# Kernel tuning notes

Hardware: AMD Instinct MI355X
Metric: run time of the kernel (lower is better)

## Reference

```python
import jax, jax.numpy as jnp
import numpy as np

N_EMBD = 768
N_HEAD = 12
HEAD_DIM = N_EMBD // N_HEAD  # 64


def setup_inputs() -> dict:
    key = jax.random.key(0)
    k1, k2, k3 = jax.random.split(key, 3)
    B, S = 4, 2048
    x = jax.random.normal(k1, (B, S, N_EMBD), dtype=jnp.float32)
    W_attn = jax.random.normal(k2, (N_EMBD, 3 * N_EMBD), dtype=jnp.float32) * 0.02
    b_attn = jax.random.normal(k3, (3 * N_EMBD,), dtype=jnp.float32) * 0.02
    return {"x": x, "W_attn": W_attn, "b_attn": b_attn}


def reference(x, W_attn, b_attn):
    B, S, E = x.shape
    H, D = N_HEAD, HEAD_DIM
    # fused QKV projection (torch Linear: x @ W^T + b; here W_attn stored as [E, 3E])
    qkv = x @ W_attn + b_attn  # [B, S, 3E]
    q, k, v = jnp.split(qkv, 3, axis=-1)
    q = q.reshape(B, S, H, D)
    k = k.reshape(B, S, H, D)
    v = v.reshape(B, S, H, D)
    scale = 1.0 / np.sqrt(D).astype(np.float32)
    scores = jnp.einsum('bqhd,bkhd->bhqk', q, k) * scale  # [B, H, S, S]
    causal = jnp.tril(jnp.ones((S, S), dtype=bool))
    # ReLU attention nonlinearity (no softmax); masked entries -> 0
    att = jnp.where(causal, jnp.maximum(scores, 0.0), 0.0)
    y = jnp.einsum('bhqk,bkhd->bqhd', att, v)  # [B, S, H, D]
    return y.reshape(B, S, E)
```

## Files before the change

### kernel.cpp

```cpp
#include <hip/hip_runtime.h>

typedef __attribute__((ext_vector_type(8))) short short8;
typedef __attribute__((ext_vector_type(4))) short short4v;
typedef __attribute__((ext_vector_type(4))) float floatx4;
typedef __attribute__((ext_vector_type(2))) unsigned int uint2v;

#define S_LEN 2048
#define NH 12
#define HD 64
#define EMB 768
#define E3 2304
#define N_ITEMS 768

__device__ __forceinline__ unsigned short f2bf(float f) {
    unsigned int u = __builtin_bit_cast(unsigned int, f);
    u += 0x7FFFu + ((u >> 16) & 1u);
    return (unsigned short)(u >> 16);
}

__device__ __forceinline__ unsigned int pack2bf(float a, float b) {
#if __has_builtin(__builtin_amdgcn_cvt_pk_bf16_f32)
    typedef __attribute__((ext_vector_type(2))) short short2v;
    short2v r = __builtin_amdgcn_cvt_pk_bf16_f32(a, b);
    return __builtin_bit_cast(unsigned int, r);
#else
    return (unsigned int)f2bf(a) | ((unsigned int)f2bf(b) << 16);
#endif
}

__device__ __forceinline__ void gl_lds16(const void* g, void* l) {
    __builtin_amdgcn_global_load_lds(
        (const __attribute__((address_space(1))) unsigned int*)g,
        (__attribute__((address_space(3))) unsigned int*)l, 16, 0, 0);
}

__global__ __launch_bounds__(256) void conv_x(const float* __restrict__ x,
                                              ushort* __restrict__ xb,
                                              int* __restrict__ counter) {
    if (blockIdx.x == 0 && threadIdx.x == 0) *counter = 0;
    int i = (blockIdx.x * 256 + threadIdx.x) * 4;
    float4 f = *(const float4*)(x + i);
    ushort4 o;
    o.x = f2bf(f.x); o.y = f2bf(f.y); o.z = f2bf(f.z); o.w = f2bf(f.w);
    *(ushort4*)(xb + i) = o;
}

__global__ __launch_bounds__(256) void conv_w(const float* __restrict__ W,
                                              ushort* __restrict__ Wt) {
    __shared__ float tile[32][33];
    int n0 = blockIdx.x * 32, k0 = blockIdx.y * 32;
    int tx = threadIdx.x, ty = threadIdx.y;
    for (int i = 0; i < 4; i++)
        tile[ty + i * 8][tx] = W[(size_t)(k0 + ty + i * 8) * E3 + n0 + tx];
    __syncthreads();
    for (int i = 0; i < 4; i++)
        Wt[(size_t)(n0 + ty + i * 8) * EMB + k0 + tx] = f2bf(tile[tx][ty + i * 8]);
}

__global__ __launch_bounds__(256) void qkv_gemm(const ushort* __restrict__ Xb,
                                                const ushort* __restrict__ Wt,
                                                const float* __restrict__ bias,
                                                ushort* __restrict__ Q,
                                                ushort* __restrict__ K,
                                                ushort* __restrict__ Vt) {
    __shared__ ushort Ald[128 * 64];
    __shared__ ushort Bld[128 * 64];
    int tid  = threadIdx.x;
    int wv = tid >> 6, lane = tid & 63;
    int l15 = lane & 15, quad = lane >> 4;
    int r8 = lane >> 3, cc = lane & 7;
    int wm = wv >> 1, wn = wv & 1;
    int m0 = blockIdx.x * 128, n0 = blockIdx.y * 128;

    floatx4 acc[4][4] = {};

    for (int k0 = 0; k0 < EMB; k0 += 64) {
        __syncthreads();
        for (int i = 0; i < 4; i++) {
            int row = wv * 32 + i * 8 + r8;
            int gc  = cc ^ r8;
            gl_lds16(Xb + (size_t)(m0 + row) * EMB + k0 + gc * 8,
                     (char*)Ald + (wv * 32 + i * 8) * 128);
            gl_lds16(Wt + (size_t)(n0 + row) * EMB + k0 + gc * 8,
                     (char*)Bld + (wv * 32 + i * 8) * 128);
        }
        __syncthreads();
        for (int ch = 0; ch < 2; ch++) {
            int sw = ((ch * 4 + quad) ^ (l15 & 7)) * 16;
            short8 af[4], bf[4];
            for (int mi = 0; mi < 4; mi++)
                af[mi] = *(const short8*)((const char*)Ald + (wm * 64 + mi * 16 + l15) * 128 + sw);
            for (int ni = 0; ni < 4; ni++)
                bf[ni] = *(const short8*)((const char*)Bld + (wn * 64 + ni * 16 + l15) * 128 + sw);
            for (int mi = 0; mi < 4; mi++)
                for (int ni = 0; ni < 4; ni++)
                    acc[mi][ni] = __builtin_amdgcn_mfma_f32_16x16x32_bf16(
                        af[mi], bf[ni], acc[mi][ni], 0, 0, 0);
        }
    }

    int seg = n0 / EMB;
    for (int ni = 0; ni < 4; ni++) {
        int n = n0 + wn * 64 + ni * 16 + l15;
        float bv = bias[n];
        int nn = n - seg * EMB;
        int h = nn >> 6, d = nn & 63;
        for (int mi = 0; mi < 4; mi++) {
            for (int r = 0; r < 4; r++) {
                int m = m0 + wm * 64 + mi * 16 + quad * 4 + r;
                int b = m >> 11, s = m & 2047;
                ushort v = f2bf(acc[mi][ni][r] + bv);
                if (seg == 0)
                    Q[(((size_t)b * NH + h) * S_LEN + s) * HD + d] = v;
                else if (seg == 1)
                    K[(((size_t)b * NH + h) * S_LEN + s) * HD + d] = v;
                else
                    Vt[(((size_t)b * NH + h) * HD + d) * S_LEN + s] = v;
            }
        }
    }
}

__global__ __launch_bounds__(256) void attn(const ushort* __restrict__ Q,
                                            const ushort* __restrict__ K,
                                            const ushort* __restrict__ Vt,
                                            float* __restrict__ out,
                                            int* __restrict__ counter) {
    __shared__ ushort Kld[2][64 * 64];
    __shared__ ushort Vld[2][64 * 64];
    __shared__ int s_item;
    int tid = threadIdx.x;
    int w = tid >> 6, lane = tid & 63;
    int l15 = lane & 15, quad = lane >> 4;
    int r8 = lane >> 3, cc = lane & 7;

    while (true) {
        if (tid == 0) s_item = atomicAdd(counter, 1);
        __syncthreads();
        int it = s_item;
        __syncthreads();
        if (it >= N_ITEMS) break;
        int qt = 15 - it / 48;
        int bh = it % 48;

        const ushort* Qbase = Q + ((size_t)bh * S_LEN + qt * 128) * HD;
        const ushort* Kbase = K + (size_t)bh * S_LEN * HD;
        const ushort* Vbase = Vt + (size_t)bh * HD * S_LEN;

        short8 qf[2][2];
        for (int nq = 0; nq < 2; nq++)
            for (int ch = 0; ch < 2; ch++)
                qf[nq][ch] = *(const short8*)(Qbase + (size_t)(w * 32 + nq * 16 + l15) * HD
                                              + ch * 32 + quad * 8);

        floatx4 acco[2][4] = {};
        int njt = 2 * qt + 2;

        {
            const ushort* Kt = Kbase;
            const ushort* Vb = Vbase;
            for (int i = 0; i < 2; i++) {
                int row = w * 16 + i * 8 + r8;
                int gc  = cc ^ r8;
                gl_lds16(Kt + (size_t)row * HD + gc * 8,
                         (char*)Kld[0] + (w * 16 + i * 8) * 128);
                gl_lds16(Vb + (size_t)row * S_LEN + gc * 8,
                         (char*)Vld[0] + (w * 16 + i * 8) * 128);
            }
        }
        int p = 0;
        for (int jt = 0; jt < njt; jt++) {
            __syncthreads();
            if (jt + 1 < njt) {
                const ushort* Kt = Kbase + (size_t)(jt + 1) * 64 * HD;
                const ushort* Vb = Vbase + (size_t)(jt + 1) * 64;
                for (int i = 0; i < 2; i++) {
                    int row = w * 16 + i * 8 + r8;
                    int gc  = cc ^ r8;
                    gl_lds16(Kt + (size_t)row * HD + gc * 8,
                             (char*)Kld[p ^ 1] + (w * 16 + i * 8) * 128);
                    gl_lds16(Vb + (size_t)row * S_LEN + gc * 8,
                             (char*)Vld[p ^ 1] + (w * 16 + i * 8) * 128);
                }
            }

            floatx4 st[4][2] = {};
            for (int ch = 0; ch < 2; ch++) {
                int sw = ((ch * 4 + quad) ^ (l15 & 7)) * 16;
                short8 kf[4];
                for (int mk = 0; mk < 4; mk++)
                    kf[mk] = *(const short8*)((const char*)Kld[p] + (mk * 16 + l15) * 128 + sw);
                for (int mk = 0; mk < 4; mk++)
                    for (int nq = 0; nq < 2; nq++)
                        st[mk][nq] = __builtin_amdgcn_mfma_f32_16x16x32_bf16(
                            kf[mk], qf[nq][ch], st[mk][nq], 0, 0, 0);
            }

            unsigned int pk[4][2][2];
            bool diag = (jt >= 2 * qt);
            for (int mk = 0; mk < 4; mk++) {
                for (int nq = 0; nq < 2; nq++) {
                    float e[4];
                    for (int r = 0; r < 4; r++)
                        e[r] = fmaxf(st[mk][nq][r] * 0.125f, 0.0f);
                    if (diag) {
                        int kg = jt * 64 + mk * 16 + quad * 4;
                        int qg = qt * 128 + w * 32 + nq * 16 + l15;
                        for (int r = 0; r < 4; r++)
                            if (kg + r > qg) e[r] = 0.0f;
                    }
                    pk[mk][nq][0] = pack2bf(e[0], e[1]);
                    pk[mk][nq][1] = pack2bf(e[2], e[3]);
                }
            }

            for (int mk = 0; mk < 4; mk++) {
                short4v vf[4];
                for (int ni = 0; ni < 4; ni++) {
                    int c2 = (mk * 2 + (quad >> 1)) ^ (l15 & 7);
                    vf[ni] = *(const short4v*)((const char*)Vld[p] + (ni * 16 + l15) * 128
                                               + c2 * 16 + (quad & 1) * 8);
                }
                for (int mi = 0; mi < 2; mi++) {
                    short4v a = __builtin_bit_cast(short4v,
                                 (uint2v){pk[mk][mi][0], pk[mk][mi][1]});
                    for (int ni = 0; ni < 4; ni++)
                        acco[mi][ni] = __builtin_amdgcn_mfma_f32_16x16x16bf16_1k(
                            a, vf[ni], acco[mi][ni], 0, 0, 0);
                }
            }
            p ^= 1;
        }

        int b = bh / NH, h = bh % NH;
        for (int mi = 0; mi < 2; mi++) {
            for (int ni = 0; ni < 4; ni++) {
                int d = ni * 16 + l15;
                for (int r = 0; r < 4; r++) {
                    int s = qt * 128 + w * 32 + mi * 16 + quad * 4 + r;
                    out[((size_t)(b * S_LEN + s)) * EMB + h * HD + d] = acco[mi][ni][r];
                }
            }
        }
        __syncthreads();
    }
}

extern "C" void kernel_launch(void* const* d_in, const int* in_sizes, int n_in,
                              void* d_out, int out_size, void* d_ws, size_t ws_size,
                              hipStream_t stream) {
    const float* x    = (const float*)d_in[0];
    const float* W    = (const float*)d_in[1];
    const float* bias = (const float*)d_in[2];
    float* out = (float*)d_out;

    char* ws = (char*)d_ws;
    const size_t SZ_X = (size_t)8192 * EMB * 2;
    const size_t SZ_W = (size_t)E3 * EMB * 2;
    const size_t SZ_H = (size_t)4 * NH * S_LEN * HD * 2;
    ushort* Xb = (ushort*)(ws);
    ushort* Wt = (ushort*)(ws + SZ_X);
    ushort* Qb = (ushort*)(ws + SZ_X + SZ_W);
    ushort* Kb = (ushort*)(ws + SZ_X + SZ_W + SZ_H);
    ushort* Vt = (ushort*)(ws + SZ_X + SZ_W + 2 * SZ_H);
    int* counter = (int*)(ws + SZ_X + SZ_W + 3 * SZ_H);

    conv_x<<<dim3(8192 * EMB / (256 * 4)), dim3(256), 0, stream>>>(x, Xb, counter);
    conv_w<<<dim3(E3 / 32, EMB / 32), dim3(32, 8), 0, stream>>>(W, Wt);
    qkv_gemm<<<dim3(64, 18), dim3(256), 0, stream>>>(Xb, Wt, bias, Qb, Kb, Vt);
    attn<<<dim3(512), dim3(256), 0, stream>>>(Qb, Kb, Vt, out, counter);
}
```

Before: 202.8 us.

## Fuse conversion kernels, stage GEMM epilogue through LDS, use 128-key attention tiles

Merges the x and W bf16 conversion kernels into one launch. The QKV GEMM epilogue now goes through LDS so it can write coalesced 16-byte stores, with Q pre-scaled by 1/8 into a token-major QK buffer and V transposed per tile. The attention loop processes 128-key stages with larger double-buffered K/V tiles, halving the barrier count, and reads Q and K straight from the row-major QK buffer with a stride of 1536. The cost is more LDS per block, which may lower occupancy, and strided global reads for K.

After: 187.6 us. 1.08x faster.

```diff
diff --git a/kernel.cpp b/kernel.cpp
--- a/kernel.cpp
+++ b/kernel.cpp
@@ -34,37 +34,40 @@
         (__attribute__((address_space(3))) unsigned int*)l, 16, 0, 0);
 }
 
-__global__ __launch_bounds__(256) void conv_x(const float* __restrict__ x,
-                                              ushort* __restrict__ xb,
-                                              int* __restrict__ counter) {
-    if (blockIdx.x == 0 && threadIdx.x == 0) *counter = 0;
-    int i = (blockIdx.x * 256 + threadIdx.x) * 4;
-    float4 f = *(const float4*)(x + i);
-    ushort4 o;
-    o.x = f2bf(f.x); o.y = f2bf(f.y); o.z = f2bf(f.z); o.w = f2bf(f.w);
-    *(ushort4*)(xb + i) = o;
-}
-
-__global__ __launch_bounds__(256) void conv_w(const float* __restrict__ W,
-                                              ushort* __restrict__ Wt) {
-    __shared__ float tile[32][33];
-    int n0 = blockIdx.x * 32, k0 = blockIdx.y * 32;
-    int tx = threadIdx.x, ty = threadIdx.y;
-    for (int i = 0; i < 4; i++)
-        tile[ty + i * 8][tx] = W[(size_t)(k0 + ty + i * 8) * E3 + n0 + tx];
-    __syncthreads();
-    for (int i = 0; i < 4; i++)
-        Wt[(size_t)(n0 + ty + i * 8) * EMB + k0 + tx] = f2bf(tile[tx][ty + i * 8]);
+__global__ __launch_bounds__(256) void conv_fused(const float* __restrict__ x,
+                                                  ushort* __restrict__ xb,
+                                                  const float* __restrict__ W,
+                                                  ushort* __restrict__ Wt,
+                                                  int* __restrict__ counter) {
+    int tid = threadIdx.x;
+    if (blockIdx.x == 0 && tid == 0) *counter = 0;
+    if (blockIdx.x < 6144) {
+        int i = (blockIdx.x * 256 + tid) * 4;
+        float4 f = *(const float4*)(x + i);
+        ushort4 o;
+        o.x = f2bf(f.x); o.y = f2bf(f.y); o.z = f2bf(f.z); o.w = f2bf(f.w);
+        *(ushort4*)(xb + i) = o;
+    } else {
+        __shared__ float tile[32][33];
+        int b2 = blockIdx.x - 6144;
+        int n0 = (b2 % 72) * 32, k0 = (b2 / 72) * 32;
+        int tx = tid & 31, ty = tid >> 5;
+        for (int i = 0; i < 4; i++)
+            tile[ty + i * 8][tx] = W[(size_t)(k0 + ty + i * 8) * E3 + n0 + tx];
+        __syncthreads();
+        for (int i = 0; i < 4; i++)
+            Wt[(size_t)(n0 + ty + i * 8) * EMB + k0 + tx] = f2bf(tile[tx][ty + i * 8]);
+    }
 }
 
 __global__ __launch_bounds__(256) void qkv_gemm(const ushort* __restrict__ Xb,
                                                 const ushort* __restrict__ Wt,
                                                 const float* __restrict__ bias,
-                                                ushort* __restrict__ Q,
-                                                ushort* __restrict__ K,
+                                                ushort* __restrict__ QKb,
                                                 ushort* __restrict__ Vt) {
-    __shared__ ushort Ald[128 * 64];
-    __shared__ ushort Bld[128 * 64];
+    __shared__ ushort lds[33792 / 2];
+    ushort* Ald = lds;
+    ushort* Bld = lds + 128 * 64;
     int tid  = threadIdx.x;
     int wv = tid >> 6, lane = tid & 63;
     int l15 = lane & 15, quad = lane >> 4;
@@ -99,150 +102,181 @@
         }
     }
 
-    int seg = n0 / EMB;
-    for (int ni = 0; ni < 4; ni++) {
-        int n = n0 + wn * 64 + ni * 16 + l15;
-        float bv = bias[n];
-        int nn = n - seg * EMB;
+    __syncthreads();
+    if (n0 < 1536) {
+        float scale = (n0 < 768) ? 0.125f : 1.0f;
+        for (int ni = 0; ni < 4; ni++) {
+            int nl = wn * 64 + ni * 16 + l15;
+            float bv = bias[n0 + nl];
+            for (int mi = 0; mi < 4; mi++)
+                for (int r = 0; r < 4; r++) {
+                    int ml = wm * 64 + mi * 16 + quad * 4 + r;
+                    lds[ml * 132 + nl] = f2bf((acc[mi][ni][r] + bv) * scale);
+                }
+        }
+        __syncthreads();
+        int row = tid >> 1, half = tid & 1;
+        size_t gm = (size_t)(m0 + row);
+        for (int i = 0; i < 8; i++) {
+            uint4 v = *(const uint4*)&lds[row * 132 + half * 64 + i * 8];
+            *(uint4*)&QKb[gm * 1536 + n0 + half * 64 + i * 8] = v;
+        }
+    } else {
+        for (int ni = 0; ni < 4; ni++) {
+            int nl = wn * 64 + ni * 16 + l15;
+            float bv = bias[n0 + nl];
+            for (int mi = 0; mi < 4; mi++) {
+                int ml = wm * 64 + mi * 16 + quad * 4;
+                ushort4 pk4;
+                pk4.x = f2bf(acc[mi][ni][0] + bv);
+                pk4.y = f2bf(acc[mi][ni][1] + bv);
+                pk4.z = f2bf(acc[mi][ni][2] + bv);
+                pk4.w = f2bf(acc[mi][ni][3] + bv);
+                *(ushort4*)&lds[nl * 132 + ml] = pk4;
+            }
+        }
+        __syncthreads();
+        int row = tid >> 1, half = tid & 1;
+        int nn = n0 + row - 1536;
         int h = nn >> 6, d = nn & 63;
-        for (int mi = 0; mi < 4; mi++) {
-            for (int r = 0; r < 4; r++) {
-                int m = m0 + wm * 64 + mi * 16 + quad * 4 + r;
-                int b = m >> 11, s = m & 2047;
-                ushort v = f2bf(acc[mi][ni][r] + bv);
-                if (seg == 0)
-                    Q[(((size_t)b * NH + h) * S_LEN + s) * HD + d] = v;
-                else if (seg == 1)
-                    K[(((size_t)b * NH + h) * S_LEN + s) * HD + d] = v;
-                else
-                    Vt[(((size_t)b * NH + h) * HD + d) * S_LEN + s] = v;
-            }
+        int b = m0 >> 11, s0 = m0 & 2047;
+        for (int i = 0; i < 8; i++) {
+            uint4 v = *(const uint4*)&lds[row * 132 + half * 64 + i * 8];
+            *(uint4*)&Vt[((size_t)(b * NH + h) * 64 + d) * S_LEN + s0 + half * 64 + i * 8] = v;
         }
     }
 }
 
-__global__ __launch_bounds__(256) void attn(const ushort* __restrict__ Q,
-                                            const ushort* __restrict__ K,
+__global__ __launch_bounds__(256) void attn(const ushort* __restrict__ QKb,
                                             const ushort* __restrict__ Vt,
                                             float* __restrict__ out,
                                             int* __restrict__ counter) {
-    __shared__ ushort Kld[2][64 * 64];
-    __shared__ ushort Vld[2][64 * 64];
-    __shared__ int s_item;
+    __shared__ ushort Kld[2][128 * 64];
+    __shared__ ushort Vld[2][64 * 128];
+    int* slot = (int*)&Kld[0][0];
     int tid = threadIdx.x;
     int w = tid >> 6, lane = tid & 63;
     int l15 = lane & 15, quad = lane >> 4;
     int r8 = lane >> 3, cc = lane & 7;
 
     while (true) {
-        if (tid == 0) s_item = atomicAdd(counter, 1);
-        __syncthreads();
-        int it = s_item;
+        __syncthreads();
+        if (tid == 0) *slot = atomicAdd(counter, 1);
+        __syncthreads();
+        int it = *slot;
         __syncthreads();
         if (it >= N_ITEMS) break;
         int qt = 15 - it / 48;
         int bh = it % 48;
-
-        const ushort* Qbase = Q + ((size_t)bh * S_LEN + qt * 128) * HD;
-        const ushort* Kbase = K + (size_t)bh * S_LEN * HD;
+        int bg = bh / NH, h = bh % NH;
+
+        const ushort* Qcol = QKb + (size_t)bg * S_LEN * 1536 + h * 64;
+        const ushort* Kcol = QKb + (size_t)bg * S_LEN * 1536 + 768 + h * 64;
         const ushort* Vbase = Vt + (size_t)bh * HD * S_LEN;
 
         short8 qf[2][2];
         for (int nq = 0; nq < 2; nq++)
             for (int ch = 0; ch < 2; ch++)
-                qf[nq][ch] = *(const short8*)(Qbase + (size_t)(w * 32 + nq * 16 + l15) * HD
-                                              + ch * 32 + quad * 8);
+                qf[nq][ch] = *(const short8*)(Qcol +
+                    (size_t)(qt * 128 + w * 32 + nq * 16 + l15) * 1536 + ch * 32 + quad * 8);
 
         floatx4 acco[2][4] = {};
-        int njt = 2 * qt + 2;
+        int nst = qt + 1;
 
         {
-            const ushort* Kt = Kbase;
-            const ushort* Vb = Vbase;
-            for (int i = 0; i < 2; i++) {
-                int row = w * 16 + i * 8 + r8;
-                int gc  = cc ^ r8;
-                gl_lds16(Kt + (size_t)row * HD + gc * 8,
-                         (char*)Kld[0] + (w * 16 + i * 8) * 128);
-                gl_lds16(Vb + (size_t)row * S_LEN + gc * 8,
-                         (char*)Vld[0] + (w * 16 + i * 8) * 128);
-            }
-        }
+            for (int i = 0; i < 4; i++) {
+                int rK = w * 32 + i * 8;
+                gl_lds16(Kcol + (size_t)(rK + r8) * 1536 + (cc ^ r8) * 8,
+                         (char*)Kld[0] + rK * 128);
+            }
+            for (int i = 0; i < 4; i++) {
+                int rV = w * 16 + i * 4;
+                int rr = lane >> 4;
+                int gc = (lane & 15) ^ ((i * 4 + rr) & 15);
+                gl_lds16(Vbase + (size_t)(rV + rr) * S_LEN + gc * 8,
+                         (char*)Vld[0] + rV * 256);
+            }
+        }
+
         int p = 0;
-        for (int jt = 0; jt < njt; jt++) {
+        for (int st_i = 0; st_i < nst; st_i++) {
             __syncthreads();
-            if (jt + 1 < njt) {
-                const ushort* Kt = Kbase + (size_t)(jt + 1) * 64 * HD;
-                const ushort* Vb = Vbase + (size_t)(jt + 1) * 64;
-                for (int i = 0; i < 2; i++) {
-                    int row = w * 16 + i * 8 + r8;
-                    int gc  = cc ^ r8;
-                    gl_lds16(Kt + (size_t)row * HD + gc * 8,
-                             (char*)Kld[p ^ 1] + (w * 16 + i * 8) * 128);
-                    gl_lds16(Vb + (size_t)row * S_LEN + gc * 8,
-                             (char*)Vld[p ^ 1] + (w * 16 + i * 8) * 128);
-                }
-            }
-
-            floatx4 st[4][2] = {};
-            for (int ch = 0; ch < 2; ch++) {
-                int sw = ((ch * 4 + quad) ^ (l15 & 7)) * 16;
-                short8 kf[4];
-                for (int mk = 0; mk < 4; mk++)
-                    kf[mk] = *(const short8*)((const char*)Kld[p] + (mk * 16 + l15) * 128 + sw);
-                for (int mk = 0; mk < 4; mk++)
-                    for (int nq = 0; nq < 2; nq++)
-                        st[mk][nq] = __builtin_amdgcn_mfma_f32_16x16x32_bf16(
-                            kf[mk], qf[nq][ch], st[mk][nq], 0, 0, 0);
-            }
-
-            unsigned int pk[4][2][2];
-            bool diag = (jt >= 2 * qt);
-            for (int mk = 0; mk < 4; mk++) {
-                for (int nq = 0; nq < 2; nq++) {
-                    float e[4];
-                    for (int r = 0; r < 4; r++)
-                        e[r] = fmaxf(st[mk][nq][r] * 0.125f, 0.0f);
-                    if (diag) {
-                        int kg = jt * 64 + mk * 16 + quad * 4;
-                        int qg = qt * 128 + w * 32 + nq * 16 + l15;
+            if (st_i + 1 < nst) {
+                const ushort* Kc = Kcol + (size_t)(st_i + 1) * 128 * 1536;
+                const ushort* Vc = Vbase + (size_t)(st_i + 1) * 128;
+                for (int i = 0; i < 4; i++) {
+                    int rK = w * 32 + i * 8;
+                    gl_lds16(Kc + (size_t)(rK + r8) * 1536 + (cc ^ r8) * 8,
+                             (char*)Kld[p ^ 1] + rK * 128);
+                }
+                for (int i = 0; i < 4; i++) {
+                    int rV = w * 16 + i * 4;
+                    int rr = lane >> 4;
+                    int gc = (lane & 15) ^ ((i * 4 + rr) & 15);
+                    gl_lds16(Vc + (size_t)(rV + rr) * S_LEN + gc * 8,
+                             (char*)Vld[p ^ 1] + rV * 256);
+                }
+            }
+            bool diag = (st_i == qt);
+
+            for (int jsub = 0; jsub < 2; jsub++) {
+                floatx4 st[4][2] = {};
+                for (int ch = 0; ch < 2; ch++) {
+                    int sw = ((ch * 4 + quad) ^ (l15 & 7)) * 16;
+                    short8 kf[4];
+                    for (int mk = 0; mk < 4; mk++)
+                        kf[mk] = *(const short8*)((const char*)Kld[p] +
+                                  (jsub * 64 + mk * 16 + l15) * 128 + sw);
+                    for (int mk = 0; mk < 4; mk++)
+                        for (int nq = 0; nq < 2; nq++)
+                            st[mk][nq] = __builtin_amdgcn_mfma_f32_16x16x32_bf16(
+                                kf[mk], qf[nq][ch], st[mk][nq], 0, 0, 0);
+                }
+
+                unsigned int pk[4][2][2];
+                for (int mk = 0; mk < 4; mk++) {
+                    for (int nq = 0; nq < 2; nq++) {
+                        float e[4];
                         for (int r = 0; r < 4; r++)
-                            if (kg + r > qg) e[r] = 0.0f;
+                            e[r] = fmaxf(st[mk][nq][r], 0.0f);
+                        if (diag) {
+                            int kg = (st_i * 2 + jsub) * 64 + mk * 16 + quad * 4;
+                            int qg = qt * 128 + w * 32 + nq * 16 + l15;
+                            for (int r = 0; r < 4; r++)
+                                if (kg + r > qg) e[r] = 0.0f;
+                        }
+                        pk[mk][nq][0] = pack2bf(e[0], e[1]);
+                        pk[mk][nq][1] = pack2bf(e[2], e[3]);
                     }
-                    pk[mk][nq][0] = pack2bf(e[0], e[1]);
-                    pk[mk][nq][1] = pack2bf(e[2], e[3]);
-                }
-            }
-
-            for (int mk = 0; mk < 4; mk++) {
-                short4v vf[4];
-                for (int ni = 0; ni < 4; ni++) {
-                    int c2 = (mk * 2 + (quad >> 1)) ^ (l15 & 7);
-                    vf[ni] = *(const short4v*)((const char*)Vld[p] + (ni * 16 + l15) * 128
-                                               + c2 * 16 + (quad & 1) * 8);
-                }
-                for (int mi = 0; mi < 2; mi++) {
-                    short4v a = __builtin_bit_cast(short4v,
-                                 (uint2v){pk[mk][mi][0], pk[mk][mi][1]});
+                }
+
+                for (int mk = 0; mk < 4; mk++) {
+                    int u = jsub * 8 + mk * 2 + (quad >> 1);
+                    short4v vf[4];
                     for (int ni = 0; ni < 4; ni++)
-                        acco[mi][ni] = __builtin_amdgcn_mfma_f32_16x16x16bf16_1k(
-                            a, vf[ni], acco[mi][ni], 0, 0, 0);
+                        vf[ni] = *(const short4v*)((const char*)Vld[p] +
+                                  (ni * 16 + l15) * 256 + (u ^ l15) * 16 + (quad & 1) * 8);
+                    for (int mi = 0; mi < 2; mi++) {
+                        short4v a = __builtin_bit_cast(short4v,
+                                     (uint2v){pk[mk][mi][0], pk[mk][mi][1]});
+                        for (int ni = 0; ni < 4; ni++)
+                            acco[mi][ni] = __builtin_amdgcn_mfma_f32_16x16x16bf16_1k(
+                                a, vf[ni], acco[mi][ni], 0, 0, 0);
+                    }
                 }
             }
             p ^= 1;
         }
 
-        int b = bh / NH, h = bh % NH;
         for (int mi = 0; mi < 2; mi++) {
             for (int ni = 0; ni < 4; ni++) {
                 int d = ni * 16 + l15;
                 for (int r = 0; r < 4; r++) {
                     int s = qt * 128 + w * 32 + mi * 16 + quad * 4 + r;
-                    out[((size_t)(b * S_LEN + s)) * EMB + h * HD + d] = acco[mi][ni][r];
-                }
-            }
-        }
-        __syncthreads();
+                    out[((size_t)bg * S_LEN + s) * EMB + h * 64 + d] = acco[mi][ni][r];
+                }
+            }
+        }
     }
 }
 
@@ -255,18 +289,17 @@
     float* out = (float*)d_out;
 
     char* ws = (char*)d_ws;
-    const size_t SZ_X = (size_t)8192 * EMB * 2;
-    const size_t SZ_W = (size_t)E3 * EMB * 2;
-    const size_t SZ_H = (size_t)4 * NH * S_LEN * HD * 2;
-    ushort* Xb = (ushort*)(ws);
-    ushort* Wt = (ushort*)(ws + SZ_X);
-    ushort* Qb = (ushort*)(ws + SZ_X + SZ_W);
-    ushort* Kb = (ushort*)(ws + SZ_X + SZ_W + SZ_H);
-    ushort* Vt = (ushort*)(ws + SZ_X + SZ_W + 2 * SZ_H);
-    int* counter = (int*)(ws + SZ_X + SZ_W + 3 * SZ_H);
-
-    conv_x<<<dim3(8192 * EMB / (256 * 4)), dim3(256), 0, stream>>>(x, Xb, counter);
-    conv_w<<<dim3(E3 / 32, EMB / 32), dim3(32, 8), 0, stream>>>(W, Wt);
-    qkv_gemm<<<dim3(64, 18), dim3(256), 0, stream>>>(Xb, Wt, bias, Qb, Kb, Vt);
-    attn<<<dim3(512), dim3(256), 0, stream>>>(Qb, Kb, Vt, out, counter);
-}
+    const size_t SZ_X  = (size_t)8192 * EMB * 2;
+    const size_t SZ_W  = (size_t)E3 * EMB * 2;
+    const size_t SZ_QK = (size_t)8192 * 1536 * 2;
+    const size_t SZ_V  = (size_t)48 * HD * S_LEN * 2;
+    ushort* Xb  = (ushort*)(ws);
+    ushort* Wt  = (ushort*)(ws + SZ_X);
+    ushort* QKb = (ushort*)(ws + SZ_X + SZ_W);
+    ushort* Vt  = (ushort*)(ws + SZ_X + SZ_W + SZ_QK);
+    int* counter = (int*)(ws + SZ_X + SZ_W + SZ_QK + SZ_V);
+
+    conv_fused<<<dim3(6144 + 1728), dim3(256), 0, stream>>>(x, Xb, W, Wt, counter);
+    qkv_gemm<<<dim3(64, 18), dim3(256), 0, stream>>>(Xb, Wt, bias, QKb, Vt);
+    attn<<<dim3(512), dim3(256), 0, stream>>>(QKb, Vt, out, counter);
+}
```
